# Optimization experiments

Measured on AMD Instinct MI355X. Metric: run time of the kernel, lower is better.

The kernel has to match this reference:

```python
import jax, jax.numpy as jnp
import numpy as np

N_NODES = 50000
N_EDGES = 800000
IN_DIM = 8
EDGE_DIM = 4
HIDDEN = 16
OUT_DIM = 1


def _lin_init(key, fan_in, fan_out):
    kw, kb = jax.random.split(key)
    bound = 1.0 / np.sqrt(fan_in)
    W = jax.random.uniform(kw, (fan_in, fan_out), minval=-bound, maxval=bound, dtype=jnp.float32)
    b = jax.random.uniform(kb, (fan_out,), minval=-bound, maxval=bound, dtype=jnp.float32)
    return W, b


def setup_inputs() -> dict:
    key = jax.random.key(0)
    ks = jax.random.split(key, 16)
    x = jax.random.normal(ks[0], (N_NODES, IN_DIM), dtype=jnp.float32)
    edge_index = jax.random.randint(ks[1], (2, N_EDGES), 0, N_NODES, dtype=jnp.int32)
    edge_attr = jax.random.normal(ks[2], (N_EDGES, EDGE_DIM), dtype=jnp.float32)

    inp = {"x": x, "edge_index": edge_index, "edge_attr": edge_attr}
    in_dims = [IN_DIM, HIDDEN]
    for i in range(2):
        d_in = in_dims[i]
        W1, b1 = _lin_init(ks[3 + 4 * i], EDGE_DIM, HIDDEN)
        W2, b2 = _lin_init(ks[4 + 4 * i], HIDDEN, d_in * HIDDEN)
        root = jax.random.uniform(ks[5 + 4 * i], (d_in, HIDDEN), minval=-1.0 / np.sqrt(d_in), maxval=1.0 / np.sqrt(d_in), dtype=jnp.float32)
        bias = jnp.zeros((HIDDEN,), dtype=jnp.float32)
        inp[f"eW1_{i}"] = W1; inp[f"eb1_{i}"] = b1
        inp[f"eW2_{i}"] = W2; inp[f"eb2_{i}"] = b2
        inp[f"root_{i}"] = root; inp[f"bias_{i}"] = bias
    mW1, mb1 = _lin_init(ks[11], HIDDEN, HIDDEN)
    mW2, mb2 = _lin_init(ks[12], HIDDEN, OUT_DIM)
    inp["mW1"] = mW1; inp["mb1"] = mb1; inp["mW2"] = mW2; inp["mb2"] = mb2
    return inp


def _nnconv(x, src, dst, edge_attr, eW1, eb1, eW2, eb2, root, bias):
    # edge MLP -> per-edge weight matrix [E, d_in, HIDDEN]
    h = jax.nn.silu(edge_attr @ eW1 + eb1)
    Wedge = (h @ eW2 + eb2).reshape(edge_attr.shape[0], x.shape[1], HIDDEN)
    # gather source features, per-edge matmul, scatter-mean to targets
    msg = jnp.einsum('ei,eio->eo', x[src], Wedge)  # [E, HIDDEN]
    agg = jax.ops.segment_sum(msg, dst, num_segments=N_NODES)
    cnt = jax.ops.segment_sum(jnp.ones((msg.shape[0],), dtype=msg.dtype), dst, num_segments=N_NODES)
    agg = agg / jnp.maximum(cnt, 1.0)[:, None]
    return x @ root + agg + bias


def reference(x, edge_index, edge_attr,
              eW1_0, eb1_0, eW2_0, eb2_0, root_0, bias_0,
              eW1_1, eb1_1, eW2_1, eb2_1, root_1, bias_1,
              mW1, mb1, mW2, mb2):
    src, dst = edge_index[0], edge_index[1]
    x = jax.nn.relu(_nnconv(x, src, dst, edge_attr, eW1_0, eb1_0, eW2_0, eb2_0, root_0, bias_0))
    x = jax.nn.relu(_nnconv(x, src, dst, edge_attr, eW1_1, eb1_1, eW2_1, eb2_1, root_1, bias_1))
    out = jax.nn.sigmoid(jax.nn.silu(x @ mW1 + mb1) @ mW2 + mb2)
    return out
```

## Files before the change

kernel.cpp:

```cpp
#include <hip/hip_runtime.h>
#include <hip/hip_fp16.h>

#define NN 50000
#define NE 800000

__device__ __forceinline__ float sigm(float v) { return 1.0f / (1.0f + __expf(-v)); }

__global__ void scan_k1(const int* __restrict__ cnt, int n, int* __restrict__ bsum)
{
    __shared__ int s[256];
    int t = threadIdx.x;
    int base = blockIdx.x * 2048 + t * 8;
    int sum = 0;
#pragma unroll
    for (int q = 0; q < 8; ++q) { int idx = base + q; if (idx < n) sum += cnt[idx]; }
    s[t] = sum;
    __syncthreads();
#pragma unroll
    for (int d = 128; d; d >>= 1) { if (t < d) s[t] += s[t + d]; __syncthreads(); }
    if (t == 0) bsum[blockIdx.x] = s[0];
}

__global__ void scan_k3(const int* __restrict__ cnt, int n,
                        const int* __restrict__ bsum, int nb,
                        int* __restrict__ offset)
{
    __shared__ int s[256];
    __shared__ int sb[64];
    int t = threadIdx.x;
    if (t < 64) sb[t] = (t < nb) ? bsum[t] : 0;
    int base = blockIdx.x * 2048 + t * 8;
    int v[8]; int sum = 0;
#pragma unroll
    for (int q = 0; q < 8; ++q) {
        int idx = base + q;
        v[q] = (idx < n) ? cnt[idx] : 0;
        sum += v[q];
    }
    s[t] = sum;
    __syncthreads();
    if (t == 0) {
        int run = 0;
        for (int i = 0; i < nb; ++i) { int x = sb[i]; sb[i] = run; run += x; }
    }
#pragma unroll
    for (int d = 1; d < 256; d <<= 1) {
        int a = (t >= d) ? s[t - d] : 0;
        __syncthreads();
        s[t] += a;
        __syncthreads();
    }
    int run = sb[blockIdx.x] + ((t > 0) ? s[t - 1] : 0);
#pragma unroll
    for (int q = 0; q < 8; ++q) {
        int idx = base + q;
        if (idx <= n) offset[idx] = run;
        run += v[q];
    }
}

__global__ void build_ranks(const int* __restrict__ ei,
                            int* __restrict__ cnt,
                            unsigned short* __restrict__ rank_s,
                            unsigned short* __restrict__ rank_d)
{
    int e = blockIdx.x * 256 + threadIdx.x;
    int s = ei[e], d = ei[NE + e];
    rank_d[e] = (unsigned short)atomicAdd(cnt + d, 1);
    rank_s[e] = (unsigned short)atomicAdd(cnt + NN + s, 1);
}

__global__ void build_perm(const int* __restrict__ ei,
                           const int* __restrict__ off_all,
                           const unsigned short* __restrict__ rank_s,
                           const unsigned short* __restrict__ rank_d,
                           unsigned long long* __restrict__ sperm64)
{
    int e = blockIdx.x * 256 + threadIdx.x;
    int s = ei[e], d = ei[NE + e];
    int spos = off_all[NN + s] - NE + (int)rank_s[e];
    int dp   = off_all[d] + (int)rank_d[e];
    sperm64[spos] = ((unsigned long long)(s & 15) << 40)
                  | ((unsigned long long)(unsigned)dp << 20)
                  | (unsigned long long)(unsigned)e;
}

template<int DIN>
__global__ __launch_bounds__(256) void edge_fusedG(
        const float* __restrict__ xin,
        const unsigned long long* __restrict__ sperm64,
        const float* __restrict__ ea,
        const float* __restrict__ eW1,
        const float* __restrict__ eb1,
        const float* __restrict__ eW2,
        const float* __restrict__ eb2,
        const int*   __restrict__ off_all,
        __half* __restrict__ msgbuf)
{
    constexpr int MROW = 260;
    constexpr int W2B  = DIN * 16 * 20 * 4;
    constexpr int SMB  = 16 * MROW * 4 + 256 * 4;
    constexpr int UNIB = (W2B > SMB) ? W2B : SMB;
    __shared__ __align__(16) char uni[UNIB];
    float* w2L   = (float*)uni;
    float* smemM = (float*)uni;
    int*   sdp   = (int*)(uni + 16 * MROW * 4);
    __shared__ __align__(16) float4 G4[16 * 69];
    __shared__ __align__(16) float4 xbL[16 * 5];
    __shared__ __align__(16) float  xL[16 * DIN];
    __shared__ __align__(16) float  b2L[DIN * 16];
    __shared__ __align__(16) float4 w1t[16];
    __shared__ __align__(16) float  b1s[16];

    int tid = threadIdx.x;
    int nb  = blockIdx.x * 16;
    if (tid < 16) {
        w1t[tid] = make_float4(eW1[tid], eW1[16 + tid], eW1[32 + tid], eW1[48 + tid]);
        b1s[tid] = eb1[tid];
    }
    for (int t = tid; t < 16 * DIN * 16; t += 256) {
        int k = t / (DIN * 16);
        int rem = t - k * DIN * 16;
        int i = rem >> 4, o = rem & 15;
        w2L[(i * 16 + k) * 20 + o] = eW2[t];
    }
    for (int t = tid; t < DIN * 16; t += 256) b2L[t] = eb2[t];
    for (int t = tid; t < 16 * DIN; t += 256) xL[t] = xin[(size_t)nb * DIN + t];
    __syncthreads();

    {
        int nl = tid >> 4, k = tid & 15;
        const float* xrow = xL + nl * DIN;
#pragma unroll
        for (int ob = 0; ob < 4; ++ob) {
            float4 a4 = make_float4(0.f, 0.f, 0.f, 0.f);
#pragma unroll
            for (int i = 0; i < DIN; ++i) {
                const float4 w = *((const float4*)(w2L + (i * 16 + k) * 20) + ob);
                a4.x += xrow[i] * w.x; a4.y += xrow[i] * w.y;
                a4.z += xrow[i] * w.z; a4.w += xrow[i] * w.w;
            }
            G4[nl * 69 + ob * 17 + k] = a4;
        }
        if (k < 4) {
            int ob = k;
            const float4* b2v = (const float4*)b2L;
            float4 a4 = make_float4(0.f, 0.f, 0.f, 0.f);
#pragma unroll
            for (int i = 0; i < DIN; ++i) {
                float4 b = b2v[i * 4 + ob];
                a4.x += xrow[i] * b.x; a4.y += xrow[i] * b.y;
                a4.z += xrow[i] * b.z; a4.w += xrow[i] * b.w;
            }
            xbL[nl * 5 + ob] = a4;
        }
    }
    __syncthreads();

    int eBeg = off_all[NN + nb] - NE;
    int eEnd = off_all[NN + nb + 16] - NE;
    for (int cb = eBeg; cb < eEnd; cb += 256) {
        int pos = cb + tid;
        bool valid = pos < eEnd;
        unsigned long long pk = valid ? sperm64[pos] : 0ull;
        int e  = (int)(pk & 0xFFFFFu);
        int dp = (int)((pk >> 20) & 0xFFFFFu);
        int sl = (int)(pk >> 40);
        float4 a = valid ? ((const float4*)ea)[e] : make_float4(0.f, 0.f, 0.f, 0.f);

        float h[16];
#pragma unroll
        for (int j = 0; j < 16; ++j) {
            float4 w = w1t[j];
            float p = b1s[j] + a.x * w.x + a.y * w.y + a.z * w.z + a.w * w.w;
            h[j] = p * sigm(p);
        }
        float4 acc[4];
#pragma unroll
        for (int ob = 0; ob < 4; ++ob) acc[ob] = xbL[sl * 5 + ob];
#pragma unroll
        for (int k = 0; k < 16; ++k) {
            float hk = h[k];
#pragma unroll
            for (int ob = 0; ob < 4; ++ob) {
                float4 g = G4[sl * 69 + ob * 17 + k];
                acc[ob].x += hk * g.x; acc[ob].y += hk * g.y;
                acc[ob].z += hk * g.z; acc[ob].w += hk * g.w;
            }
        }
        sdp[tid] = valid ? dp : -1;
#pragma unroll
        for (int ob = 0; ob < 4; ++ob) {
            smemM[(ob * 4 + 0) * MROW + tid] = acc[ob].x;
            smemM[(ob * 4 + 1) * MROW + tid] = acc[ob].y;
            smemM[(ob * 4 + 2) * MROW + tid] = acc[ob].z;
            smemM[(ob * 4 + 3) * MROW + tid] = acc[ob].w;
        }
        __syncthreads();
#pragma unroll
        for (int r = 0; r < 8; ++r) {
            int le = r * 32 + (tid >> 3);
            int p  = tid & 7;
            int d2 = sdp[le];
            float v0 = smemM[(2 * p)     * MROW + le];
            float v1 = smemM[(2 * p + 1) * MROW + le];
            if (d2 >= 0) {
                __half2 hv = __floats2half2_rn(v0, v1);
                *((__half2*)(msgbuf + (size_t)d2 * 16) + p) = hv;
            }
        }
        __syncthreads();
    }
}

__device__ __forceinline__ float gather_msg16(const __half* __restrict__ msgbuf,
                                              int s0, int e0, int tid)
{
    int half = (tid >> 3) & 1;
    int p    = tid & 7;
    float ax = 0.f, ay = 0.f;
    for (int j = s0 + half; j < e0; j += 2) {
        __half2 hv = *((const __half2*)(msgbuf + (size_t)j * 16) + p);
        float2 f = __half22float2(hv);
        ax += f.x; ay += f.y;
    }
    ax += __shfl_xor(ax, 8, 16);
    ay += __shfl_xor(ay, 8, 16);
    int ch = tid & 15;
    float vx = __shfl(ax, ch >> 1, 16);
    float vy = __shfl(ay, ch >> 1, 16);
    return (ch & 1) ? vy : vx;
}

__global__ __launch_bounds__(256) void gather_L0(
        const float* __restrict__ xin,
        const float* __restrict__ root,
        const float* __restrict__ bias,
        const int*   __restrict__ off_all,
        const __half* __restrict__ msgbuf,
        float* __restrict__ x1)
{
    __shared__ __align__(16) float rootL[8 * 16];
    __shared__ __align__(16) float biasL[16];
    int tid = threadIdx.x;
    if (tid < 128) rootL[tid] = root[tid];
    if (tid < 16) biasL[tid] = bias[tid];
    __syncthreads();

    int ch = tid & 15;
    int n  = blockIdx.x * 16 + (tid >> 4);
    int s0 = off_all[n], e0 = off_all[n + 1];

    float acc = gather_msg16(msgbuf, s0, e0, tid);
    float v = acc / fmaxf((float)(e0 - s0), 1.0f) + biasL[ch];
#pragma unroll
    for (int i = 0; i < 8; ++i)
        v += xin[(size_t)n * 8 + i] * rootL[i * 16 + ch];
    x1[(size_t)n * 16 + ch] = fmaxf(v, 0.f);
}

__global__ __launch_bounds__(256) void gather_final(
        const float* __restrict__ x1,
        const float* __restrict__ root,
        const float* __restrict__ bias,
        const int*   __restrict__ off_all,
        const __half* __restrict__ msgbuf,
        const float* __restrict__ mW1,
        const float* __restrict__ mb1,
        const float* __restrict__ mW2,
        const float* __restrict__ mb2,
        float* __restrict__ out)
{
    __shared__ __align__(16) float rootL[256];
    __shared__ __align__(16) float biasL[16];
    __shared__ __align__(16) float w1m[256];
    __shared__ __align__(16) float b1m[16];
    __shared__ __align__(16) float w2m[16];
    __shared__ float b2m;
    int tid = threadIdx.x;
    rootL[tid] = root[tid];
    w1m[tid] = mW1[tid];
    if (tid < 16) { biasL[tid] = bias[tid]; b1m[tid] = mb1[tid]; w2m[tid] = mW2[tid]; }
    if (tid == 0) b2m = mb2[0];
    __syncthreads();

    int ch = tid & 15;
    int n  = blockIdx.x * 16 + (tid >> 4);
    int s0 = off_all[n], e0 = off_all[n + 1];

    float acc = gather_msg16(msgbuf, s0, e0, tid);
    float v = acc / fmaxf((float)(e0 - s0), 1.0f) + biasL[ch];
#pragma unroll
    for (int i = 0; i < 16; ++i)
        v += x1[(size_t)n * 16 + i] * rootL[i * 16 + ch];
    v = fmaxf(v, 0.f);

    float z = b1m[ch];
#pragma unroll
    for (int o = 0; o < 16; ++o) {
        float vo = __shfl(v, o, 16);
        z += vo * w1m[o * 16 + ch];
    }
    float ss = z * sigm(z) * w2m[ch];
#pragma unroll
    for (int off = 8; off; off >>= 1) ss += __shfl_xor(ss, off, 16);
    if (ch == 0) out[n] = sigm(ss + b2m);
}

extern "C" void kernel_launch(void* const* d_in, const int* in_sizes, int n_in,
                              void* d_out, int out_size, void* d_ws, size_t ws_size,
                              hipStream_t stream) {
    const float* x     = (const float*)d_in[0];
    const int*   ei    = (const int*)  d_in[1];
    const float* ea    = (const float*)d_in[2];
    const float* eW1_0 = (const float*)d_in[3];
    const float* eb1_0 = (const float*)d_in[4];
    const float* eW2_0 = (const float*)d_in[5];
    const float* eb2_0 = (const float*)d_in[6];
    const float* root0 = (const float*)d_in[7];
    const float* bias0 = (const float*)d_in[8];
    const float* eW1_1 = (const float*)d_in[9];
    const float* eb1_1 = (const float*)d_in[10];
    const float* eW2_1 = (const float*)d_in[11];
    const float* eb2_1 = (const float*)d_in[12];
    const float* root1 = (const float*)d_in[13];
    const float* bias1 = (const float*)d_in[14];
    const float* mW1   = (const float*)d_in[15];
    const float* mb1   = (const float*)d_in[16];
    const float* mW2   = (const float*)d_in[17];
    const float* mb2   = (const float*)d_in[18];
    float* out = (float*)d_out;

    const int EG = NE / 256;
    const int GG = NN / 16;
    const int SN = 2 * NN;
    const int SB = (SN + 2047) / 2048;

    int* W = (int*)d_ws;
    int*   off_all = W;
    int*   bsum    = W + 100004;
    unsigned short* rank_s = (unsigned short*)(W + 100516);
    unsigned short* rank_d = (unsigned short*)(W + 500516);
    unsigned long long* sperm64 = (unsigned long long*)(W + 900516);
    float*  x1     = (float*)(W + 2500516);
    __half* msgbuf = (__half*)(W + 3300516);
    int*    cnt    = W + 3300516;

    hipMemsetAsync(cnt, 0, SN * sizeof(int), stream);
    build_ranks<<<EG, 256, 0, stream>>>(ei, cnt, rank_s, rank_d);
    scan_k1<<<SB, 256, 0, stream>>>(cnt, SN, bsum);
    scan_k3<<<SB, 256, 0, stream>>>(cnt, SN, bsum, SB, off_all);
    build_perm<<<EG, 256, 0, stream>>>(ei, off_all, rank_s, rank_d, sperm64);

    edge_fusedG<8><<<GG, 256, 0, stream>>>(x, sperm64, ea, eW1_0, eb1_0,
                                           eW2_0, eb2_0, off_all, msgbuf);
    gather_L0<<<GG, 256, 0, stream>>>(x, root0, bias0, off_all, msgbuf, x1);

    edge_fusedG<16><<<GG, 256, 0, stream>>>(x1, sperm64, ea, eW1_1, eb1_1,
                                            eW2_1, eb2_1, off_all, msgbuf);
    gather_final<<<GG, 256, 0, stream>>>(x1, root1, bias1, off_all, msgbuf,
                                         mW1, mb1, mW2, mb2, out);
}
```

Measured before the change: 300.6 us.

## Privatize degree-count atomics per XCD and merge per-XCD offsets in scan

Each XCD now increments its own copy of the src/dst degree counters, using workgroup-scope relaxed atomics, and the XCD id is packed into the 16-bit rank. scan_k1 turns the per-XCD counts into exclusive per-XCD prefixes and totals. build_perm adds the per-XCD prefix back when computing the final CSR position. The aim is to avoid device-wide atomic contention and cross-XCD coherence traffic when building the CSR. The cost is an eight-times larger memset, extra count reads and writes in the scan, one extra gather in build_perm, and a cap of 4096 on per-XCD ranks.

```diff
diff --git a/kernel.cpp b/kernel.cpp
--- a/kernel.cpp
+++ b/kernel.cpp
@@ -3,22 +3,57 @@
 
 #define NN 50000
 #define NE 800000
+#define SN (2 * NN)
+#define NXCD 8
 
 __device__ __forceinline__ float sigm(float v) { return 1.0f / (1.0f + __expf(-v)); }
 
-__global__ void scan_k1(const int* __restrict__ cnt, int n, int* __restrict__ bsum)
-{
-    __shared__ int s[256];
+__global__ void build_ranks(const int* __restrict__ ei,
+                            int* __restrict__ cntX,
+                            unsigned short* __restrict__ rank_s,
+                            unsigned short* __restrict__ rank_d)
+{
+    unsigned xcd;
+    asm volatile("s_getreg_b32 %0, hwreg(HW_REG_XCC_ID, 0, 32)" : "=s"(xcd));
+    xcd &= 7;
+    int e = blockIdx.x * 256 + threadIdx.x;
+    int s = ei[e], d = ei[NE + e];
+    int* base = cntX + xcd * SN;
+    unsigned rd = (unsigned)__hip_atomic_fetch_add(base + d, 1,
+                        __ATOMIC_RELAXED, __HIP_MEMORY_SCOPE_WORKGROUP);
+    unsigned rs = (unsigned)__hip_atomic_fetch_add(base + NN + s, 1,
+                        __ATOMIC_RELAXED, __HIP_MEMORY_SCOPE_WORKGROUP);
+    rank_d[e] = (unsigned short)((xcd << 12) | rd);
+    rank_s[e] = (unsigned short)((xcd << 12) | rs);
+}
+
+__global__ void scan_k1(int* __restrict__ cntX, int* __restrict__ cnt_tot,
+                        int n, int* __restrict__ bsum)
+{
+    __shared__ int sm[256];
     int t = threadIdx.x;
-    int base = blockIdx.x * 2048 + t * 8;
+    int base = blockIdx.x * 2048;
     int sum = 0;
 #pragma unroll
-    for (int q = 0; q < 8; ++q) { int idx = base + q; if (idx < n) sum += cnt[idx]; }
-    s[t] = sum;
-    __syncthreads();
-#pragma unroll
-    for (int d = 128; d; d >>= 1) { if (t < d) s[t] += s[t + d]; __syncthreads(); }
-    if (t == 0) bsum[blockIdx.x] = s[0];
+    for (int q = 0; q < 8; ++q) {
+        int idx = base + q * 256 + t;
+        if (idx < n) {
+            int run = 0;
+#pragma unroll
+            for (int x = 0; x < NXCD; ++x) {
+                int c = cntX[x * SN + idx];
+                cntX[x * SN + idx] = run;
+                run += c;
+            }
+            cnt_tot[idx] = run;
+            sum += run;
+        }
+    }
+    sm[t] = sum;
+    __syncthreads();
+#pragma unroll
+    for (int d = 128; d; d >>= 1) { if (t < d) sm[t] += sm[t + d]; __syncthreads(); }
+    if (t == 0) bsum[blockIdx.x] = sm[0];
 }
 
 __global__ void scan_k3(const int* __restrict__ cnt, int n,
@@ -59,27 +94,20 @@
     }
 }
 
-__global__ void build_ranks(const int* __restrict__ ei,
-                            int* __restrict__ cnt,
-                            unsigned short* __restrict__ rank_s,
-                            unsigned short* __restrict__ rank_d)
-{
-    int e = blockIdx.x * 256 + threadIdx.x;
-    int s = ei[e], d = ei[NE + e];
-    rank_d[e] = (unsigned short)atomicAdd(cnt + d, 1);
-    rank_s[e] = (unsigned short)atomicAdd(cnt + NN + s, 1);
-}
-
 __global__ void build_perm(const int* __restrict__ ei,
                            const int* __restrict__ off_all,
                            const unsigned short* __restrict__ rank_s,
                            const unsigned short* __restrict__ rank_d,
+                           const int* __restrict__ cntX,
                            unsigned long long* __restrict__ sperm64)
 {
     int e = blockIdx.x * 256 + threadIdx.x;
     int s = ei[e], d = ei[NE + e];
-    int spos = off_all[NN + s] - NE + (int)rank_s[e];
-    int dp   = off_all[d] + (int)rank_d[e];
+    unsigned prs = rank_s[e], prd = rank_d[e];
+    int spos = off_all[NN + s] - NE
+             + cntX[(int)(prs >> 12) * SN + NN + s] + (int)(prs & 0xFFFu);
+    int dp   = off_all[d]
+             + cntX[(int)(prd >> 12) * SN + d]      + (int)(prd & 0xFFFu);
     sperm64[spos] = ((unsigned long long)(s & 15) << 40)
                   | ((unsigned long long)(unsigned)dp << 20)
                   | (unsigned long long)(unsigned)e;
@@ -333,7 +361,6 @@
 
     const int EG = NE / 256;
     const int GG = NN / 16;
-    const int SN = 2 * NN;
     const int SB = (SN + 2047) / 2048;
 
     int* W = (int*)d_ws;
@@ -344,13 +371,14 @@
     unsigned long long* sperm64 = (unsigned long long*)(W + 900516);
     float*  x1     = (float*)(W + 2500516);
     __half* msgbuf = (__half*)(W + 3300516);
-    int*    cnt    = W + 3300516;
-
-    hipMemsetAsync(cnt, 0, SN * sizeof(int), stream);
-    build_ranks<<<EG, 256, 0, stream>>>(ei, cnt, rank_s, rank_d);
-    scan_k1<<<SB, 256, 0, stream>>>(cnt, SN, bsum);
-    scan_k3<<<SB, 256, 0, stream>>>(cnt, SN, bsum, SB, off_all);
-    build_perm<<<EG, 256, 0, stream>>>(ei, off_all, rank_s, rank_d, sperm64);
+    int*    cntX   = W + 3300516;
+    int*    cnt_tot= W + 3300516 + NXCD * SN;
+
+    hipMemsetAsync(cntX, 0, (size_t)NXCD * SN * sizeof(int), stream);
+    build_ranks<<<EG, 256, 0, stream>>>(ei, cntX, rank_s, rank_d);
+    scan_k1<<<SB, 256, 0, stream>>>(cntX, cnt_tot, SN, bsum);
+    scan_k3<<<SB, 256, 0, stream>>>(cnt_tot, SN, bsum, SB, off_all);
+    build_perm<<<EG, 256, 0, stream>>>(ei, off_all, rank_s, rank_d, cntX, sperm64);
 
     edge_fusedG<8><<<GG, 256, 0, stream>>>(x, sperm64, ea, eW1_0, eb1_0,
                                            eW2_0, eb2_0, off_all, msgbuf);
```

After: 307.2 us. +2.2%, slower.

## Replace atomic rank-based CSR build with two-pass bucketed counting sort

Applied to the files above, without the earlier changes.

Replaces the per-edge global atomic ranking, two-level scan and permutation kernels with a two-level radix-style sort. Edges are first bucketed by the high bits of the destination, then locally sorted in shared memory, and the same is repeated for the source keyed by destination position. The aim is to remove heavy global atomic contention on 100K counters and scattered writes. In exchange it adds more kernel launches and extra intermediate record buffers, and ordering within each node now depends on atomic scheduling.

```diff
diff --git a/kernel.cpp b/kernel.cpp
--- a/kernel.cpp
+++ b/kernel.cpp
@@ -3,86 +3,200 @@
 
 #define NN 50000
 #define NE 800000
+#define NBUCK 196
 
 __device__ __forceinline__ float sigm(float v) { return 1.0f / (1.0f + __expf(-v)); }
 
-__global__ void scan_k1(const int* __restrict__ cnt, int n, int* __restrict__ bsum)
-{
-    __shared__ int s[256];
-    int t = threadIdx.x;
-    int base = blockIdx.x * 2048 + t * 8;
-    int sum = 0;
-#pragma unroll
-    for (int q = 0; q < 8; ++q) { int idx = base + q; if (idx < n) sum += cnt[idx]; }
-    s[t] = sum;
-    __syncthreads();
-#pragma unroll
-    for (int d = 128; d; d >>= 1) { if (t < d) s[t] += s[t + d]; __syncthreads(); }
-    if (t == 0) bsum[blockIdx.x] = s[0];
-}
-
-__global__ void scan_k3(const int* __restrict__ cnt, int n,
-                        const int* __restrict__ bsum, int nb,
-                        int* __restrict__ offset)
-{
-    __shared__ int s[256];
-    __shared__ int sb[64];
-    int t = threadIdx.x;
-    if (t < 64) sb[t] = (t < nb) ? bsum[t] : 0;
-    int base = blockIdx.x * 2048 + t * 8;
-    int v[8]; int sum = 0;
-#pragma unroll
-    for (int q = 0; q < 8; ++q) {
-        int idx = base + q;
-        v[q] = (idx < n) ? cnt[idx] : 0;
-        sum += v[q];
-    }
-    s[t] = sum;
-    __syncthreads();
-    if (t == 0) {
-        int run = 0;
-        for (int i = 0; i < nb; ++i) { int x = sb[i]; sb[i] = run; run += x; }
-    }
-#pragma unroll
-    for (int d = 1; d < 256; d <<= 1) {
-        int a = (t >= d) ? s[t - d] : 0;
-        __syncthreads();
-        s[t] += a;
-        __syncthreads();
-    }
-    int run = sb[blockIdx.x] + ((t > 0) ? s[t - 1] : 0);
-#pragma unroll
-    for (int q = 0; q < 8; ++q) {
-        int idx = base + q;
-        if (idx <= n) offset[idx] = run;
-        run += v[q];
-    }
-}
-
-__global__ void build_ranks(const int* __restrict__ ei,
-                            int* __restrict__ cnt,
-                            unsigned short* __restrict__ rank_s,
-                            unsigned short* __restrict__ rank_d)
-{
-    int e = blockIdx.x * 256 + threadIdx.x;
-    int s = ei[e], d = ei[NE + e];
-    rank_d[e] = (unsigned short)atomicAdd(cnt + d, 1);
-    rank_s[e] = (unsigned short)atomicAdd(cnt + NN + s, 1);
-}
-
-__global__ void build_perm(const int* __restrict__ ei,
-                           const int* __restrict__ off_all,
-                           const unsigned short* __restrict__ rank_s,
-                           const unsigned short* __restrict__ rank_d,
-                           unsigned long long* __restrict__ sperm64)
-{
-    int e = blockIdx.x * 256 + threadIdx.x;
-    int s = ei[e], d = ei[NE + e];
-    int spos = off_all[NN + s] - NE + (int)rank_s[e];
-    int dp   = off_all[d] + (int)rank_d[e];
-    sperm64[spos] = ((unsigned long long)(s & 15) << 40)
-                  | ((unsigned long long)(unsigned)dp << 20)
-                  | (unsigned long long)(unsigned)e;
+
+__global__ void sort_count(const int* __restrict__ ei,
+                           int* __restrict__ cntA, int* __restrict__ cntB)
+{
+    __shared__ int hA[NBUCK], hB[NBUCK];
+    int t = threadIdx.x;
+    for (int i = t; i < NBUCK; i += 256) { hA[i] = 0; hB[i] = 0; }
+    __syncthreads();
+    int base = blockIdx.x * 2048;
+#pragma unroll
+    for (int r = 0; r < 8; ++r) {
+        int idx = base + r * 256 + t;
+        if (idx < NE) {
+            int s = ei[idx], d = ei[NE + idx];
+            atomicAdd(&hB[s >> 8], 1);
+            atomicAdd(&hA[d >> 8], 1);
+        }
+    }
+    __syncthreads();
+    for (int i = t; i < NBUCK; i += 256) {
+        if (hA[i]) atomicAdd(&cntA[i], hA[i]);
+        if (hB[i]) atomicAdd(&cntB[i], hB[i]);
+    }
+}
+
+__global__ void sort_scan(const int* __restrict__ cntA, const int* __restrict__ cntB,
+                          int* __restrict__ baseA, int* __restrict__ baseB,
+                          int* __restrict__ curA,  int* __restrict__ curB)
+{
+    __shared__ int a[256], b[256];
+    int t = threadIdx.x;
+    a[t] = (t < NBUCK) ? cntA[t] : 0;
+    b[t] = (t < NBUCK) ? cntB[t] : 0;
+    __syncthreads();
+#pragma unroll
+    for (int dd = 1; dd < 256; dd <<= 1) {
+        int av = (t >= dd) ? a[t - dd] : 0;
+        int bv = (t >= dd) ? b[t - dd] : 0;
+        __syncthreads();
+        a[t] += av; b[t] += bv;
+        __syncthreads();
+    }
+    int exA = (t > 0) ? a[t - 1] : 0;
+    int exB = (t > 0) ? b[t - 1] : 0;
+    if (t < NBUCK) { baseA[t] = exA; curA[t] = exA; baseB[t] = exB; curB[t] = exB; }
+    if (t == 255)  { baseA[NBUCK] = a[255]; baseB[NBUCK] = b[255]; }
+}
+
+__global__ __launch_bounds__(256) void sort_scatterA(const int* __restrict__ ei,
+                                                     int* __restrict__ curA,
+                                                     unsigned* __restrict__ recA)
+{
+    __shared__ int lcnt[NBUCK];
+    __shared__ int lofs[NBUCK];
+    int t = threadIdx.x;
+    for (int i = t; i < NBUCK; i += 256) lcnt[i] = 0;
+    __syncthreads();
+    int base = blockIdx.x * 2048;
+#pragma unroll
+    for (int r = 0; r < 8; ++r) {
+        int e = base + r * 256 + t;
+        if (e < NE) atomicAdd(&lcnt[ei[NE + e] >> 8], 1);
+    }
+    __syncthreads();
+    for (int i = t; i < NBUCK; i += 256)
+        lofs[i] = lcnt[i] ? atomicAdd(&curA[i], lcnt[i]) : 0;
+    __syncthreads();
+#pragma unroll
+    for (int r = 0; r < 8; ++r) {
+        int e = base + r * 256 + t;
+        if (e < NE) {
+            int d = ei[NE + e];
+            int p = atomicAdd(&lofs[d >> 8], 1);
+            recA[p] = ((unsigned)(d & 255) << 20) | (unsigned)e;
+        }
+    }
+}
+
+__global__ __launch_bounds__(256) void sort_localA(const unsigned* __restrict__ recA,
+                                                   const int* __restrict__ baseA,
+                                                   int* __restrict__ off_all,
+                                                   unsigned* __restrict__ dlist)
+{
+    __shared__ int c[256];
+    __shared__ int live[256];
+    int t = threadIdx.x;
+    int b = blockIdx.x;
+    int lo = baseA[b], hi = baseA[b + 1];
+    c[t] = 0;
+    __syncthreads();
+    for (int i = lo + t; i < hi; i += 256)
+        atomicAdd(&c[(recA[i] >> 20) & 255], 1);
+    __syncthreads();
+#pragma unroll
+    for (int dd = 1; dd < 256; dd <<= 1) {
+        int v = (t >= dd) ? c[t - dd] : 0;
+        __syncthreads();
+        c[t] += v;
+        __syncthreads();
+    }
+    int ex = (t > 0) ? c[t - 1] : 0;
+    int d = (b << 8) + t;
+    if (d <= NN) off_all[d] = lo + ex;
+    live[t] = lo + ex;
+    __syncthreads();
+    for (int i = lo + t; i < hi; i += 256) {
+        unsigned rec = recA[i];
+        int pos = atomicAdd(&live[(rec >> 20) & 255], 1);
+        dlist[pos] = rec & 0xFFFFFu;
+    }
+}
+
+__global__ __launch_bounds__(256) void sort_scatterB(const int* __restrict__ ei,
+                                                     const unsigned* __restrict__ dlist,
+                                                     int* __restrict__ curB,
+                                                     unsigned long long* __restrict__ recB)
+{
+    __shared__ int lcnt[NBUCK];
+    __shared__ int lofs[NBUCK];
+    __shared__ unsigned short sS[2048];
+    __shared__ unsigned eS[2048];
+    int t = threadIdx.x;
+    for (int i = t; i < NBUCK; i += 256) lcnt[i] = 0;
+    __syncthreads();
+    int base = blockIdx.x * 2048;
+#pragma unroll
+    for (int r = 0; r < 8; ++r) {
+        int dp = base + r * 256 + t;
+        int li = r * 256 + t;
+        if (dp < NE) {
+            unsigned e = dlist[dp];
+            int s = ei[e];
+            sS[li] = (unsigned short)s;
+            eS[li] = e;
+            atomicAdd(&lcnt[s >> 8], 1);
+        }
+    }
+    __syncthreads();
+    for (int i = t; i < NBUCK; i += 256)
+        lofs[i] = lcnt[i] ? atomicAdd(&curB[i], lcnt[i]) : 0;
+    __syncthreads();
+#pragma unroll
+    for (int r = 0; r < 8; ++r) {
+        int dp = base + r * 256 + t;
+        int li = r * 256 + t;
+        if (dp < NE) {
+            int s = sS[li];
+            unsigned e = eS[li];
+            int p = atomicAdd(&lofs[s >> 8], 1);
+            recB[p] = ((unsigned long long)(s & 255) << 40)
+                    | ((unsigned long long)(unsigned)dp << 20)
+                    | (unsigned long long)e;
+        }
+    }
+}
+
+__global__ __launch_bounds__(256) void sort_localB(const unsigned long long* __restrict__ recB,
+                                                   const int* __restrict__ baseB,
+                                                   int* __restrict__ off_all,
+                                                   unsigned long long* __restrict__ sperm64)
+{
+    __shared__ int c[256];
+    __shared__ int live[256];
+    int t = threadIdx.x;
+    int b = blockIdx.x;
+    int lo = baseB[b], hi = baseB[b + 1];
+    c[t] = 0;
+    __syncthreads();
+    for (int i = lo + t; i < hi; i += 256)
+        atomicAdd(&c[(int)(recB[i] >> 40) & 255], 1);
+    __syncthreads();
+#pragma unroll
+    for (int dd = 1; dd < 256; dd <<= 1) {
+        int v = (t >= dd) ? c[t - dd] : 0;
+        __syncthreads();
+        c[t] += v;
+        __syncthreads();
+    }
+    int ex = (t > 0) ? c[t - 1] : 0;
+    int s = (b << 8) + t;
+    if (s <= NN) off_all[NN + s] = NE + lo + ex;
+    live[t] = lo + ex;
+    __syncthreads();
+    for (int i = lo + t; i < hi; i += 256) {
+        unsigned long long rec = recB[i];
+        int k = (int)(rec >> 40) & 255;
+        int pos = atomicAdd(&live[k], 1);
+        int sl = ((b << 8) + k) & 15;
+        sperm64[pos] = ((unsigned long long)sl << 40) | (rec & 0xFFFFFFFFFFull);
+    }
 }
 
 template<int DIN>
@@ -331,26 +445,31 @@
     const float* mb2   = (const float*)d_in[18];
     float* out = (float*)d_out;
 
-    const int EG = NE / 256;
-    const int GG = NN / 16;
-    const int SN = 2 * NN;
-    const int SB = (SN + 2047) / 2048;
+    const int GG  = NN / 16;
+    const int SBK = (NE + 2047) / 2048;
 
     int* W = (int*)d_ws;
-    int*   off_all = W;
-    int*   bsum    = W + 100004;
-    unsigned short* rank_s = (unsigned short*)(W + 100516);
-    unsigned short* rank_d = (unsigned short*)(W + 500516);
-    unsigned long long* sperm64 = (unsigned long long*)(W + 900516);
-    float*  x1     = (float*)(W + 2500516);
-    __half* msgbuf = (__half*)(W + 3300516);
-    int*    cnt    = W + 3300516;
-
-    hipMemsetAsync(cnt, 0, SN * sizeof(int), stream);
-    build_ranks<<<EG, 256, 0, stream>>>(ei, cnt, rank_s, rank_d);
-    scan_k1<<<SB, 256, 0, stream>>>(cnt, SN, bsum);
-    scan_k3<<<SB, 256, 0, stream>>>(cnt, SN, bsum, SB, off_all);
-    build_perm<<<EG, 256, 0, stream>>>(ei, off_all, rank_s, rank_d, sperm64);
+    int* off_all = W;
+    int* cntA    = W + 100004;
+    int* cntB    = W + 100260;
+    int* baseA   = W + 100516;
+    int* baseB   = W + 100716;
+    int* curA    = W + 100916;
+    int* curB    = W + 101172;
+    unsigned long long* sperm64 = (unsigned long long*)(W + 101440);
+    float*  x1     = (float*)(W + 1701440);
+    __half* msgbuf = (__half*)(W + 2501440);
+    unsigned* recA  = (unsigned*)(W + 2501440);
+    unsigned* dlist = (unsigned*)(W + 3301440);
+    unsigned long long* recB = (unsigned long long*)(W + 4101440);
+
+    hipMemsetAsync(cntA, 0, 512 * sizeof(int), stream);
+    sort_count   <<<SBK,   256, 0, stream>>>(ei, cntA, cntB);
+    sort_scan    <<<1,     256, 0, stream>>>(cntA, cntB, baseA, baseB, curA, curB);
+    sort_scatterA<<<SBK,   256, 0, stream>>>(ei, curA, recA);
+    sort_localA  <<<NBUCK, 256, 0, stream>>>(recA, baseA, off_all, dlist);
+    sort_scatterB<<<SBK,   256, 0, stream>>>(ei, dlist, curB, recB);
+    sort_localB  <<<NBUCK, 256, 0, stream>>>(recB, baseB, off_all, sperm64);
 
     edge_fusedG<8><<<GG, 256, 0, stream>>>(x, sperm64, ea, eW1_0, eb1_0,
                                            eW2_0, eb2_0, off_all, msgbuf);
```

Result: faster. 292.6 us (-2.7%).
